# Performance work log

Hardware: AMD Instinct MI355X
Metric: run time of the kernel (lower is better)

Reference implementation:

```python
import jax, jax.numpy as jnp
import numpy as np

NEG_SLOPE = 0.2  # PyG GATConv default negative_slope
EPS = 1e-16


def gat_conv(x, src, dst, num_nodes, W, a_src, a_dst, bias, heads, out_c, concat):
    """PyG-style GATConv (eval mode, self-loops already appended).
    x: [N, F_in]; src/dst: [E] (edge j->i with src=j, dst=i).
    W: [F_in, heads*out_c]; a_src/a_dst: [heads, out_c]; bias: [heads*out_c] or [out_c].
    """
    xw = (x @ W).reshape(num_nodes, heads, out_c)          # [N, H, C]
    alpha_src = jnp.sum(xw * a_src, axis=-1)               # [N, H]
    alpha_dst = jnp.sum(xw * a_dst, axis=-1)               # [N, H]
    e = jax.nn.leaky_relu(alpha_src[src] + alpha_dst[dst], NEG_SLOPE)  # [E, H]
    # numerically stable segment softmax over edges grouped by destination node
    m = jax.ops.segment_max(e, dst, num_segments=num_nodes)            # [N, H]
    e = jnp.exp(e - m[dst])
    denom = jax.ops.segment_sum(e, dst, num_segments=num_nodes)        # [N, H]
    alpha = e / (denom[dst] + EPS)                                     # [E, H]
    # weighted scatter-sum aggregation of source messages
    out = jax.ops.segment_sum(xw[src] * alpha[:, :, None], dst, num_segments=num_nodes)  # [N, H, C]
    if concat:
        out = out.reshape(num_nodes, heads * out_c)
    else:
        out = out.mean(axis=1)
    return out + bias


def setup_inputs() -> dict:
    key = jax.random.key(0)
    ks = jax.random.split(key, 12)
    N, E = 50000, 800000
    F_in, Hid, H1, Out = 512, 32, 8, 64

    def xavier(k, shape, gain=1.414):
        fan_in, fan_out = shape[0], shape[-1] if len(shape) == 2 else int(np.prod(shape[1:]))
        a = gain * np.sqrt(6.0 / (fan_in + fan_out))
        return jax.random.uniform(k, shape, jnp.float32, -a, a)

    x = jax.random.normal(ks[0], (N, F_in), jnp.float32)
    edge_index = jax.random.randint(ks[1], (2, E), 0, N, jnp.int64)

    W1 = xavier(ks[2], (F_in, H1 * Hid))
    a_src1 = xavier(ks[3], (H1, Hid))
    a_dst1 = xavier(ks[4], (H1, Hid))
    b1 = jnp.zeros((H1 * Hid,), jnp.float32)

    W2 = xavier(ks[5], (H1 * Hid, Out))
    a_src2 = xavier(ks[6], (1, Out))
    a_dst2 = xavier(ks[7], (1, Out))
    b2 = jnp.zeros((Out,), jnp.float32)

    return {"x": x, "edge_index": edge_index,
            "W1": W1, "a_src1": a_src1, "a_dst1": a_dst1, "b1": b1,
            "W2": W2, "a_src2": a_src2, "a_dst2": a_dst2, "b2": b2}


def reference(x, edge_index, W1, a_src1, a_dst1, b1, W2, a_src2, a_dst2, b2):
    N = x.shape[0]
    # add self-loops (PyG GATConv default add_self_loops=True)
    loop = jnp.arange(N, dtype=edge_index.dtype)
    src = jnp.concatenate([edge_index[0], loop])
    dst = jnp.concatenate([edge_index[1], loop])

    # eval mode: all dropouts are identity
    h = gat_conv(x, src, dst, N, W1, a_src1, a_dst1, b1, heads=8, out_c=32, concat=True)
    h = jax.nn.elu(h)
    h = gat_conv(h, src, dst, N, W2, a_src2, a_dst2, b2, heads=1, out_c=64, concat=False)
    return jax.nn.log_softmax(h, axis=1)
```

## Files before the change

kernel.cpp:

```cpp
#include <hip/hip_runtime.h>


typedef __attribute__((ext_vector_type(8)))  __bf16          bf16x8;
typedef __attribute__((ext_vector_type(8)))  unsigned short  ushort8;
typedef __attribute__((ext_vector_type(16))) float           f32x16;

#define NEG_SLOPE 0.2f
#define EPS_GAT 1e-16f

static __device__ __forceinline__ float lrelu(float x) {
    return x > 0.0f ? x : NEG_SLOPE * x;
}
static __device__ __forceinline__ unsigned short f2bf(float f) {
    unsigned u = __float_as_uint(f);
    return (unsigned short)((u + 0x7fffu + ((u >> 16) & 1u)) >> 16);
}
static __device__ __forceinline__ float bf2f(unsigned short v) {
    return __uint_as_float(((unsigned)v) << 16);
}

__global__ void k_flag(const unsigned* __restrict__ p, unsigned* sentinel, int E) {
    __shared__ int anynz;
    if (threadIdx.x == 0) anynz = 0;
    __syncthreads();
    int i = threadIdx.x;
    unsigned w = (i < E) ? p[2 * i + 1] : 0u;
    if (w != 0u) atomicOr(&anynz, 1);
    __syncthreads();
    if (threadIdx.x == 0 && anynz) *sentinel = 1u;
}

__global__ void k_convert(const void* __restrict__ p, const unsigned* __restrict__ sentinel,
                          int* __restrict__ esrc, int* __restrict__ edst,
                          int* __restrict__ counts, int E) {
    int i = blockIdx.x * 256 + threadIdx.x;
    if (i >= 2 * E) return;
    bool is64 = (*sentinel == 0u);
    int v = is64 ? (int)((const long long*)p)[i] : ((const int*)p)[i];
    if (i < E) {
        esrc[i] = v;
    } else {
        edst[i - E] = v;
        atomicAdd(&counts[v], 1);
    }
}

__global__ void k_scan1(const int* __restrict__ counts, int* __restrict__ rowp,
                        int* __restrict__ bsum, int N) {
    __shared__ int s[256];
    int t = threadIdx.x, i = blockIdx.x * 256 + t;
    int v = (i < N) ? counts[i] : 0;
    s[t] = v;
    __syncthreads();
    for (int off = 1; off < 256; off <<= 1) {
        int u = (t >= off) ? s[t - off] : 0;
        __syncthreads();
        s[t] += u;
        __syncthreads();
    }
    if (i < N) rowp[i] = s[t] - v;
    if (t == 255) bsum[blockIdx.x] = s[255];
}

__global__ void k_scan2(const int* __restrict__ bsum, int* __restrict__ boff,
                        int* __restrict__ rowp_last, int NB) {
    __shared__ int s[256];
    int t = threadIdx.x;
    int v = (t < NB) ? bsum[t] : 0;
    s[t] = v;
    __syncthreads();
    for (int off = 1; off < 256; off <<= 1) {
        int u = (t >= off) ? s[t - off] : 0;
        __syncthreads();
        s[t] += u;
        __syncthreads();
    }
    if (t < NB) boff[t] = s[t] - v;
    if (t == 255) *rowp_last = s[255];
}

__global__ void k_scan3(int* __restrict__ rowp, int* __restrict__ cursor,
                        const int* __restrict__ boff, int N) {
    int i = blockIdx.x * 256 + threadIdx.x;
    if (i < N) {
        int r = rowp[i] + boff[blockIdx.x];
        rowp[i] = r;
        cursor[i] = r;
    }
}

__global__ void k_fill(const int* __restrict__ esrc, const int* __restrict__ edst,
                       int* __restrict__ cursor, int* __restrict__ sorted_src, int E) {
    int i = blockIdx.x * 256 + threadIdx.x;
    if (i >= E) return;
    int d = edst[i];
    int pos = atomicAdd(&cursor[d], 1);
    sorted_src[pos] = esrc[i];
}

__global__ void k_prep_w(const float* __restrict__ W1, const float* __restrict__ W2,
                         unsigned short* __restrict__ w1t, unsigned short* __restrict__ w2t) {
    int t = blockIdx.x * 256 + threadIdx.x;
    if (t < 512 * 256) {
        int k = t >> 8, m = t & 255;
        w1t[m * 512 + k] = f2bf(W1[t]);
    } else {
        int u = t - 512 * 256;
        if (u < 256 * 64) {
            int k = u >> 6, m = u & 63;
            w2t[m * 256 + k] = f2bf(W2[u]);
        }
    }
}

template <int BM, int BN, int NT, bool AF32, bool OUTBF>
__global__ __launch_bounds__(NT) void k_gemm(const void* __restrict__ Ain,
                                             const unsigned short* __restrict__ Bt,
                                             void* __restrict__ Cout, int Nrows, int K) {
    constexpr int LD = 40;
    __shared__ __align__(16) unsigned short As[BM * LD];
    __shared__ __align__(16) unsigned short Bs[BN * LD];
    const int tid = threadIdx.x;
    const int blockRow = blockIdx.x * BM;
    const int wave = tid >> 6, lane = tid & 63;
    constexpr int WR = BM / 64;
    const int wr = wave % WR, wc = wave / WR;
    const int m = lane & 31;
    const int ksel = (lane >> 5) * 8;

    f32x16 acc00{}, acc01{}, acc10{}, acc11{};

    for (int kt = 0; kt < K; kt += 32) {
        if constexpr (AF32) {
            const float* A = (const float*)Ain;
            for (int idx = tid; idx < BM * 4; idx += NT) {
                int r = idx >> 2, kc = (idx & 3) * 8;
                int grow = blockRow + r;
                float v[8];
                if (grow < Nrows) {
                    const float* ap = A + (size_t)grow * K + kt + kc;
                    float4 x0 = *(const float4*)ap;
                    float4 x1 = *(const float4*)(ap + 4);
                    v[0]=x0.x; v[1]=x0.y; v[2]=x0.z; v[3]=x0.w;
                    v[4]=x1.x; v[5]=x1.y; v[6]=x1.z; v[7]=x1.w;
                } else {
                    #pragma unroll
                    for (int t = 0; t < 8; ++t) v[t] = 0.0f;
                }
                ushort8 o;
                #pragma unroll
                for (int t = 0; t < 8; ++t) o[t] = f2bf(v[t]);
                *(ushort8*)&As[r * LD + kc] = o;
            }
        } else {
            const unsigned short* A = (const unsigned short*)Ain;
            for (int idx = tid; idx < BM * 4; idx += NT) {
                int r = idx >> 2, kc = (idx & 3) * 8;
                int grow = blockRow + r;
                ushort8 o{};
                if (grow < Nrows) o = *(const ushort8*)(A + (size_t)grow * K + kt + kc);
                *(ushort8*)&As[r * LD + kc] = o;
            }
        }
        for (int idx = tid; idx < BN * 4; idx += NT) {
            int r = idx >> 2, kc = (idx & 3) * 8;
            *(ushort8*)&Bs[r * LD + kc] = *(const ushort8*)(Bt + (size_t)r * K + kt + kc);
        }
        __syncthreads();

        #pragma unroll
        for (int kk = 0; kk < 32; kk += 16) {
            bf16x8 a0 = *(const bf16x8*)&As[(wr * 64 +      m) * LD + kk + ksel];
            bf16x8 a1 = *(const bf16x8*)&As[(wr * 64 + 32 + m) * LD + kk + ksel];
            bf16x8 b0 = *(const bf16x8*)&Bs[(wc * 64 +      m) * LD + kk + ksel];
            bf16x8 b1 = *(const bf16x8*)&Bs[(wc * 64 + 32 + m) * LD + kk + ksel];
            acc00 = __builtin_amdgcn_mfma_f32_32x32x16_bf16(a0, b0, acc00, 0, 0, 0);
            acc01 = __builtin_amdgcn_mfma_f32_32x32x16_bf16(a0, b1, acc01, 0, 0, 0);
            acc10 = __builtin_amdgcn_mfma_f32_32x32x16_bf16(a1, b0, acc10, 0, 0, 0);
            acc11 = __builtin_amdgcn_mfma_f32_32x32x16_bf16(a1, b1, acc11, 0, 0, 0);
        }
        __syncthreads();
    }

    const int dcol = wc * 64 + (lane & 31);
    const int dquad = 4 * (lane >> 5);
    auto store_tile = [&](const f32x16& a, int rt, int ct) {
        #pragma unroll
        for (int r = 0; r < 16; ++r) {
            int row = blockRow + wr * 64 + rt * 32 + (r & 3) + 8 * (r >> 2) + dquad;
            if (row < Nrows) {
                size_t off = (size_t)row * BN + dcol + ct * 32;
                if constexpr (OUTBF) ((unsigned short*)Cout)[off] = f2bf(a[r]);
                else                 ((float*)Cout)[off] = a[r];
            }
        }
    };
    store_tile(acc00, 0, 0); store_tile(acc01, 0, 1);
    store_tile(acc10, 1, 0); store_tile(acc11, 1, 1);
}

__global__ void k_alpha(const unsigned short* __restrict__ xw, const float* __restrict__ a_s,
                        const float* __restrict__ a_d, float* __restrict__ os,
                        float* __restrict__ od, float* __restrict__ pmax,
                        int NH, int H, int C) {
    __shared__ float red[256];
    int t = blockIdx.x * 256 + threadIdx.x;
    float s = -1e30f, d = 0.f;
    if (t < NH) {
        int n = t / H, h = t - n * H;
        const unsigned short* row = xw + (size_t)n * H * C + h * C;
        s = 0.f;
        for (int c = 0; c < C; c += 8) {
            ushort8 v = *(const ushort8*)(row + c);
            #pragma unroll
            for (int q = 0; q < 8; ++q) {
                float f = bf2f(v[q]);
                s += f * a_s[h * C + c + q];
                d += f * a_d[h * C + c + q];
            }
        }
        os[t] = s; od[t] = d;
    }
    red[threadIdx.x] = s;
    __syncthreads();
    for (int off = 128; off >= H; off >>= 1) {
        if (threadIdx.x < off) red[threadIdx.x] = fmaxf(red[threadIdx.x], red[threadIdx.x + off]);
        __syncthreads();
    }
    if ((int)threadIdx.x < H) pmax[blockIdx.x * H + threadIdx.x] = red[threadIdx.x];
}

__global__ void k_maxred(const float* __restrict__ partial, int nB, int H,
                         float* __restrict__ M) {
    __shared__ float red[256];
    int t = threadIdx.x;
    int h = t & (H - 1);
    float m = -1e30f;
    for (int b = t / H; b < nB; b += 256 / H)
        m = fmaxf(m, partial[b * H + h]);
    red[t] = m;
    __syncthreads();
    for (int off = 128; off >= H; off >>= 1) {
        if (t < off) red[t] = fmaxf(red[t], red[t + off]);
        __syncthreads();
    }
    if (t < H) M[t] = red[t];
}

__global__ __launch_bounds__(256) void k_agg_l1(
        const unsigned short* __restrict__ xw1, const float* __restrict__ asrc,
        const float* __restrict__ adst, const float* __restrict__ Mh,
        const float* __restrict__ b1, const int* __restrict__ rp,
        const int* __restrict__ ssrc, unsigned short* __restrict__ hbf, int N) {
    int wid = (blockIdx.x * 256 + threadIdx.x) >> 6;
    if (wid >= N) return;
    int lane = threadIdx.x & 63;
    int half = lane >> 5;
    int q    = lane & 31;
    int f0   = q * 8;
    int h    = q >> 2;
    int ih   = wid * 8 + h;
    float ad = adst[ih];
    float m  = lrelu(Mh[h] + ad);
    float acc[8];
    float s;
    {
        float w = (half == 0) ? __expf(lrelu(asrc[ih] + ad) - m) : 0.0f;
        ushort8 xv = *(const ushort8*)(xw1 + (size_t)wid * 256 + f0);
        s = w;
        #pragma unroll
        for (int i = 0; i < 8; ++i) acc[i] = w * bf2f(xv[i]);
    }
    int e0 = rp[wid], e1 = rp[wid + 1];
    if (e0 < e1) {
        int ei = e0 + half;
        bool v_c = ei < e1;
        int j_c = ssrc[v_c ? ei : e1 - 1];
        float as_c = asrc[j_c * 8 + h];
        ushort8 xv_c = *(const ushort8*)(xw1 + (size_t)j_c * 256 + f0);
        for (int e = e0 + 2;; e += 2) {
            bool more = e < e1;
            bool v_n = false;
            float as_n;
            ushort8 xv_n;
            if (more) {
                int en = e + half;
                v_n = en < e1;
                int j_n = ssrc[v_n ? en : e1 - 1];
                as_n = asrc[j_n * 8 + h];
                xv_n = *(const ushort8*)(xw1 + (size_t)j_n * 256 + f0);
            }
            float w = v_c ? __expf(lrelu(as_c + ad) - m) : 0.0f;
            s += w;
            #pragma unroll
            for (int i = 0; i < 8; ++i) acc[i] += w * bf2f(xv_c[i]);
            if (!more) break;
            v_c = v_n; as_c = as_n; xv_c = xv_n;
        }
    }
    s += __shfl_xor(s, 32, 64);
    #pragma unroll
    for (int i = 0; i < 8; ++i) acc[i] += __shfl_xor(acc[i], 32, 64);
    float inv = 1.0f / (s + EPS_GAT);
    int fw = f0 + half * 4;
    ushort4 o;
    #pragma unroll
    for (int i = 0; i < 4; ++i) {
        float v = acc[half * 4 + i] * inv + b1[fw + i];
        v = v > 0.f ? v : expm1f(v);
        ((unsigned short*)&o)[i] = f2bf(v);
    }
    *(ushort4*)(hbf + (size_t)wid * 256 + fw) = o;
}

__global__ __launch_bounds__(256) void k_agg_l2(
        const unsigned short* __restrict__ xw2, const float* __restrict__ asrc,
        const float* __restrict__ adst, const float* __restrict__ Mh,
        const float* __restrict__ b2, const int* __restrict__ rp,
        const int* __restrict__ ssrc, float* __restrict__ out, int N) {
    int wid = (blockIdx.x * 256 + threadIdx.x) >> 6;
    if (wid >= N) return;
    int lane = threadIdx.x & 63;
    int g  = lane >> 4;
    int q  = lane & 15;
    int f0 = q * 4;
    float ad = adst[wid];
    float m = lrelu(Mh[0] + ad);
    float acc[4];
    float s;
    {
        float w = (g == 0) ? __expf(lrelu(asrc[wid] + ad) - m) : 0.0f;
        ushort4 xv = *(const ushort4*)(xw2 + (size_t)wid * 64 + f0);
        s = w;
        acc[0] = w * bf2f(xv.x); acc[1] = w * bf2f(xv.y);
        acc[2] = w * bf2f(xv.z); acc[3] = w * bf2f(xv.w);
    }
    int e0 = rp[wid], e1 = rp[wid + 1];
    if (e0 < e1) {
        int ei = e0 + g;
        bool v_c = ei < e1;
        int j_c = ssrc[v_c ? ei : e1 - 1];
        float as_c = asrc[j_c];
        ushort4 xv_c = *(const ushort4*)(xw2 + (size_t)j_c * 64 + f0);
        for (int e = e0 + 4;; e += 4) {
            bool more = e < e1;
            bool v_n = false;
            float as_n;
            ushort4 xv_n;
            if (more) {
                int en = e + g;
                v_n = en < e1;
                int j_n = ssrc[v_n ? en : e1 - 1];
                as_n = asrc[j_n];
                xv_n = *(const ushort4*)(xw2 + (size_t)j_n * 64 + f0);
            }
            float w = v_c ? __expf(lrelu(as_c + ad) - m) : 0.0f;
            s += w;
            acc[0] += w * bf2f(xv_c.x); acc[1] += w * bf2f(xv_c.y);
            acc[2] += w * bf2f(xv_c.z); acc[3] += w * bf2f(xv_c.w);
            if (!more) break;
            v_c = v_n; as_c = as_n; xv_c = xv_n;
        }
    }
    s += __shfl_xor(s, 16, 64);
    s += __shfl_xor(s, 32, 64);
    #pragma unroll
    for (int i = 0; i < 4; ++i) {
        acc[i] += __shfl_xor(acc[i], 16, 64);
        acc[i] += __shfl_xor(acc[i], 32, 64);
    }
    float inv = 1.0f / (s + EPS_GAT);
    float val[4];
    float mx = -1e30f;
    #pragma unroll
    for (int i = 0; i < 4; ++i) {
        val[i] = acc[i] * inv + b2[f0 + i];
        mx = fmaxf(mx, val[i]);
    }
    #pragma unroll
    for (int off = 8; off > 0; off >>= 1) mx = fmaxf(mx, __shfl_xor(mx, off, 64));
    float sm = 0.f;
    #pragma unroll
    for (int i = 0; i < 4; ++i) sm += __expf(val[i] - mx);
    #pragma unroll
    for (int off = 8; off > 0; off >>= 1) sm += __shfl_xor(sm, off, 64);
    float lse = mx + logf(sm);
    if (g == 0) {
        float4 o = make_float4(val[0] - lse, val[1] - lse, val[2] - lse, val[3] - lse);
        *(float4*)(out + (size_t)wid * 64 + f0) = o;
    }
}

static inline int cdiv(int a, int b) { return (a + b - 1) / b; }

extern "C" void kernel_launch(void* const* d_in, const int* in_sizes, int n_in,
                              void* d_out, int out_size, void* d_ws, size_t ws_size,
                              hipStream_t stream) {
    const float* x   = (const float*)d_in[0];
    const void*  eix = d_in[1];
    const float* W1  = (const float*)d_in[2];
    const float* as1 = (const float*)d_in[3];
    const float* ad1 = (const float*)d_in[4];
    const float* b1  = (const float*)d_in[5];
    const float* W2  = (const float*)d_in[6];
    const float* as2 = (const float*)d_in[7];
    const float* ad2 = (const float*)d_in[8];
    const float* b2  = (const float*)d_in[9];
    float* out = (float*)d_out;

    const int N = in_sizes[0] / 512;
    const int E = in_sizes[1] / 2;
    const int NB = cdiv(N, 256);
    const int NB1 = cdiv(N * 8, 256);
    const int NB2 = cdiv(N, 256);
    (void)n_in; (void)out_size; (void)ws_size;

    char* base = (char*)d_ws;
    size_t o = 0;
    auto alloc = [&](size_t bytes) -> char* {
        o = (o + 255) & ~(size_t)255;
        char* p = base + o;
        o += bytes;
        return p;
    };
    unsigned short* xw1b  = (unsigned short*)alloc((size_t)N * 256 * 2);
    unsigned short* hbf   = (unsigned short*)alloc((size_t)N * 256 * 2);
    unsigned short* xw2b  = (unsigned short*)alloc((size_t)N * 64 * 2);
    float*          asrc1 = (float*)alloc((size_t)N * 8 * 4);
    float*          adst1 = (float*)alloc((size_t)N * 8 * 4);
    float*          asrc2 = (float*)alloc((size_t)N * 4);
    float*          adst2 = (float*)alloc((size_t)N * 4);
    float*          pmax1 = (float*)alloc((size_t)NB1 * 8 * 4);
    float*          pmax2 = (float*)alloc((size_t)NB2 * 4);
    float*          M1    = (float*)alloc(8 * 4);
    float*          M2    = (float*)alloc(4);
    unsigned short* w1t   = (unsigned short*)alloc(512 * 256 * 2);
    unsigned short* w2t   = (unsigned short*)alloc(256 * 64 * 2);
    int*            counts= (int*)alloc((size_t)N * 4);
    int*            cursor= (int*)alloc((size_t)N * 4);
    int*            rowp  = (int*)alloc((size_t)(N + 1) * 4);
    int*            bsum  = (int*)alloc(256 * 4);
    int*            boff  = (int*)alloc(256 * 4);
    int*            esrc  = (int*)alloc((size_t)E * 4);
    int*            edst  = (int*)alloc((size_t)E * 4);
    int*            ssrc  = (int*)alloc((size_t)E * 4);
    unsigned*       sent  = (unsigned*)alloc(256);

    hipMemsetAsync(sent, 0, 4, stream);
    hipMemsetAsync(counts, 0, (size_t)N * 4, stream);

    k_flag<<<1, 256, 0, stream>>>((const unsigned*)eix, sent, E);
    k_convert<<<cdiv(2 * E, 256), 256, 0, stream>>>(eix, sent, esrc, edst, counts, E);
    k_scan1<<<NB, 256, 0, stream>>>(counts, rowp, bsum, N);
    k_scan2<<<1, 256, 0, stream>>>(bsum, boff, rowp + N, NB);
    k_scan3<<<NB, 256, 0, stream>>>(rowp, cursor, boff, N);
    k_fill<<<cdiv(E, 256), 256, 0, stream>>>(esrc, edst, cursor, ssrc, E);

    k_prep_w<<<cdiv(512 * 256 + 256 * 64, 256), 256, 0, stream>>>(W1, W2, w1t, w2t);

    k_gemm<128, 256, 512, true, true><<<cdiv(N, 128), 512, 0, stream>>>(x, w1t, xw1b, N, 512);
    k_alpha<<<NB1, 256, 0, stream>>>(xw1b, as1, ad1, asrc1, adst1, pmax1, N * 8, 8, 32);
    k_maxred<<<1, 256, 0, stream>>>(pmax1, NB1, 8, M1);
    k_agg_l1<<<cdiv(N * 64, 256), 256, 0, stream>>>(xw1b, asrc1, adst1, M1, b1,
                                                    rowp, ssrc, hbf, N);
    k_gemm<256, 64, 256, false, true><<<cdiv(N, 256), 256, 0, stream>>>(hbf, w2t, xw2b, N, 256);
    k_alpha<<<NB2, 256, 0, stream>>>(xw2b, as2, ad2, asrc2, adst2, pmax2, N, 1, 64);
    k_maxred<<<1, 256, 0, stream>>>(pmax2, NB2, 1, M2);
    k_agg_l2<<<cdiv(N * 64, 256), 256, 0, stream>>>(xw2b, asrc2, adst2, M2, b2,
                                                    rowp, ssrc, out, N);
}
```

Before: 449.1 us.

## Fuse max reduction via atomics, deepen gather prefetch, use packed bf16 conversion

Replaces the separate global-max reduction kernels with order-preserving encoded atomicMax inside the alpha kernels, removing two launches. The layer-1 aggregation now processes four edges in parallel per wave, with 16 features per lane and a two-deep prefetch of gathered rows. Layer 2 gains the same two-stage prefetch. The GEMM's fp32-to-bf16 conversion uses packed intrinsics. The deeper prefetch raises register pressure, and the extra shuffles add reduction cost.

```diff
diff --git a/kernel.cpp b/kernel.cpp
--- a/kernel.cpp
+++ b/kernel.cpp
@@ -1,4 +1,5 @@
 #include <hip/hip_runtime.h>
+#include <hip/hip_bf16.h>
 
 
 typedef __attribute__((ext_vector_type(8)))  __bf16          bf16x8;
@@ -17,6 +18,14 @@
 }
 static __device__ __forceinline__ float bf2f(unsigned short v) {
     return __uint_as_float(((unsigned)v) << 16);
+}
+static __device__ __forceinline__ unsigned encf(float x) {
+    unsigned u = __float_as_uint(x);
+    return (u >> 31) ? ~u : (u | 0x80000000u);
+}
+static __device__ __forceinline__ float decf(unsigned e) {
+    unsigned u = (e >> 31) ? (e & 0x7fffffffu) : ~e;
+    return __uint_as_float(u);
 }
 
 __global__ void k_flag(const unsigned* __restrict__ p, unsigned* sentinel, int E) {
@@ -136,21 +145,19 @@
             for (int idx = tid; idx < BM * 4; idx += NT) {
                 int r = idx >> 2, kc = (idx & 3) * 8;
                 int grow = blockRow + r;
-                float v[8];
+                union { ushort8 u; __hip_bfloat162 h[4]; } cv;
                 if (grow < Nrows) {
                     const float* ap = A + (size_t)grow * K + kt + kc;
                     float4 x0 = *(const float4*)ap;
                     float4 x1 = *(const float4*)(ap + 4);
-                    v[0]=x0.x; v[1]=x0.y; v[2]=x0.z; v[3]=x0.w;
-                    v[4]=x1.x; v[5]=x1.y; v[6]=x1.z; v[7]=x1.w;
+                    cv.h[0] = __float22bfloat162_rn(make_float2(x0.x, x0.y));
+                    cv.h[1] = __float22bfloat162_rn(make_float2(x0.z, x0.w));
+                    cv.h[2] = __float22bfloat162_rn(make_float2(x1.x, x1.y));
+                    cv.h[3] = __float22bfloat162_rn(make_float2(x1.z, x1.w));
                 } else {
-                    #pragma unroll
-                    for (int t = 0; t < 8; ++t) v[t] = 0.0f;
+                    cv.u = ushort8{};
                 }
-                ushort8 o;
-                #pragma unroll
-                for (int t = 0; t < 8; ++t) o[t] = f2bf(v[t]);
-                *(ushort8*)&As[r * LD + kc] = o;
+                *(ushort8*)&As[r * LD + kc] = cv.u;
             }
         } else {
             const unsigned short* A = (const unsigned short*)Ain;
@@ -201,7 +208,7 @@
 
 __global__ void k_alpha(const unsigned short* __restrict__ xw, const float* __restrict__ a_s,
                         const float* __restrict__ a_d, float* __restrict__ os,
-                        float* __restrict__ od, float* __restrict__ pmax,
+                        float* __restrict__ od, unsigned* __restrict__ Menc,
                         int NH, int H, int C) {
     __shared__ float red[256];
     int t = blockIdx.x * 256 + threadIdx.x;
@@ -227,86 +234,82 @@
         if (threadIdx.x < off) red[threadIdx.x] = fmaxf(red[threadIdx.x], red[threadIdx.x + off]);
         __syncthreads();
     }
-    if ((int)threadIdx.x < H) pmax[blockIdx.x * H + threadIdx.x] = red[threadIdx.x];
-}
-
-__global__ void k_maxred(const float* __restrict__ partial, int nB, int H,
-                         float* __restrict__ M) {
-    __shared__ float red[256];
-    int t = threadIdx.x;
-    int h = t & (H - 1);
-    float m = -1e30f;
-    for (int b = t / H; b < nB; b += 256 / H)
-        m = fmaxf(m, partial[b * H + h]);
-    red[t] = m;
-    __syncthreads();
-    for (int off = 128; off >= H; off >>= 1) {
-        if (t < off) red[t] = fmaxf(red[t], red[t + off]);
-        __syncthreads();
-    }
-    if (t < H) M[t] = red[t];
+    if ((int)threadIdx.x < H) atomicMax(&Menc[threadIdx.x], encf(red[threadIdx.x]));
 }
 
 __global__ __launch_bounds__(256) void k_agg_l1(
         const unsigned short* __restrict__ xw1, const float* __restrict__ asrc,
-        const float* __restrict__ adst, const float* __restrict__ Mh,
+        const float* __restrict__ adst, const unsigned* __restrict__ Menc,
         const float* __restrict__ b1, const int* __restrict__ rp,
         const int* __restrict__ ssrc, unsigned short* __restrict__ hbf, int N) {
     int wid = (blockIdx.x * 256 + threadIdx.x) >> 6;
     if (wid >= N) return;
     int lane = threadIdx.x & 63;
-    int half = lane >> 5;
-    int q    = lane & 31;
-    int f0   = q * 8;
-    int h    = q >> 2;
-    int ih   = wid * 8 + h;
+    int g  = lane >> 4;
+    int q  = lane & 15;
+    int f0 = q * 16;
+    int h  = q >> 1;
+    int ih = wid * 8 + h;
     float ad = adst[ih];
-    float m  = lrelu(Mh[h] + ad);
-    float acc[8];
+    float m  = lrelu(decf(Menc[h]) + ad);
+    float acc[16];
     float s;
     {
-        float w = (half == 0) ? __expf(lrelu(asrc[ih] + ad) - m) : 0.0f;
-        ushort8 xv = *(const ushort8*)(xw1 + (size_t)wid * 256 + f0);
+        float w = (g == 0) ? __expf(lrelu(asrc[ih] + ad) - m) : 0.0f;
+        const unsigned short* rowp_ = xw1 + (size_t)wid * 256 + f0;
+        ushort8 lo = *(const ushort8*)rowp_;
+        ushort8 hi = *(const ushort8*)(rowp_ + 8);
         s = w;
         #pragma unroll
-        for (int i = 0; i < 8; ++i) acc[i] = w * bf2f(xv[i]);
+        for (int i = 0; i < 8; ++i) { acc[i] = w * bf2f(lo[i]); acc[8 + i] = w * bf2f(hi[i]); }
     }
     int e0 = rp[wid], e1 = rp[wid + 1];
     if (e0 < e1) {
-        int ei = e0 + half;
-        bool v_c = ei < e1;
-        int j_c = ssrc[v_c ? ei : e1 - 1];
-        float as_c = asrc[j_c * 8 + h];
-        ushort8 xv_c = *(const ushort8*)(xw1 + (size_t)j_c * 256 + f0);
-        for (int e = e0 + 2;; e += 2) {
-            bool more = e < e1;
-            bool v_n = false;
-            float as_n;
-            ushort8 xv_n;
-            if (more) {
-                int en = e + half;
-                v_n = en < e1;
-                int j_n = ssrc[v_n ? en : e1 - 1];
-                as_n = asrc[j_n * 8 + h];
-                xv_n = *(const ushort8*)(xw1 + (size_t)j_n * 256 + f0);
-            }
-            float w = v_c ? __expf(lrelu(as_c + ad) - m) : 0.0f;
+        auto loadSlot = [&](int ebase, float& as, ushort8& lo, ushort8& hi, bool& val) {
+            int ei = ebase + g;
+            val = ei < e1;
+            int j = ssrc[val ? ei : e1 - 1];
+            as = asrc[j * 8 + h];
+            const unsigned short* rp_ = xw1 + (size_t)j * 256 + f0;
+            lo = *(const ushort8*)rp_;
+            hi = *(const ushort8*)(rp_ + 8);
+        };
+        float asA; ushort8 loA, hiA; bool vA;
+        loadSlot(e0, asA, loA, hiA, vA);
+        float asB = 0.f; ushort8 loB{}, hiB{}; bool vB = false;
+        bool moreB = e0 + 4 < e1;
+        if (moreB) loadSlot(e0 + 4, asB, loB, hiB, vB);
+        for (int e = e0;;) {
+            float asC = 0.f; ushort8 loC{}, hiC{}; bool vC = false;
+            bool moreC = e + 8 < e1;
+            if (moreC) loadSlot(e + 8, asC, loC, hiC, vC);
+            float w = vA ? __expf(lrelu(asA + ad) - m) : 0.0f;
             s += w;
             #pragma unroll
-            for (int i = 0; i < 8; ++i) acc[i] += w * bf2f(xv_c[i]);
-            if (!more) break;
-            v_c = v_n; as_c = as_n; xv_c = xv_n;
-        }
-    }
+            for (int i = 0; i < 8; ++i) {
+                acc[i]     += w * bf2f(loA[i]);
+                acc[8 + i] += w * bf2f(hiA[i]);
+            }
+            if (!moreB) break;
+            asA = asB; loA = loB; hiA = hiB; vA = vB;
+            asB = asC; loB = loC; hiB = hiC; vB = vC;
+            moreB = moreC;
+            e += 4;
+        }
+    }
+    s += __shfl_xor(s, 16, 64);
     s += __shfl_xor(s, 32, 64);
     #pragma unroll
-    for (int i = 0; i < 8; ++i) acc[i] += __shfl_xor(acc[i], 32, 64);
+    for (int i = 0; i < 16; ++i) {
+        acc[i] += __shfl_xor(acc[i], 16, 64);
+        acc[i] += __shfl_xor(acc[i], 32, 64);
+    }
     float inv = 1.0f / (s + EPS_GAT);
-    int fw = f0 + half * 4;
+    int fw = f0 + g * 4;
     ushort4 o;
     #pragma unroll
     for (int i = 0; i < 4; ++i) {
-        float v = acc[half * 4 + i] * inv + b1[fw + i];
+        float v = acc[g * 4 + i] * inv + b1[fw + i];
         v = v > 0.f ? v : expm1f(v);
         ((unsigned short*)&o)[i] = f2bf(v);
     }
@@ -315,7 +318,7 @@
 
 __global__ __launch_bounds__(256) void k_agg_l2(
         const unsigned short* __restrict__ xw2, const float* __restrict__ asrc,
-        const float* __restrict__ adst, const float* __restrict__ Mh,
+        const float* __restrict__ adst, const unsigned* __restrict__ Menc,
         const float* __restrict__ b2, const int* __restrict__ rp,
         const int* __restrict__ ssrc, float* __restrict__ out, int N) {
     int wid = (blockIdx.x * 256 + threadIdx.x) >> 6;
@@ -325,7 +328,7 @@
     int q  = lane & 15;
     int f0 = q * 4;
     float ad = adst[wid];
-    float m = lrelu(Mh[0] + ad);
+    float m = lrelu(decf(Menc[0]) + ad);
     float acc[4];
     float s;
     {
@@ -337,29 +340,31 @@
     }
     int e0 = rp[wid], e1 = rp[wid + 1];
     if (e0 < e1) {
-        int ei = e0 + g;
-        bool v_c = ei < e1;
-        int j_c = ssrc[v_c ? ei : e1 - 1];
-        float as_c = asrc[j_c];
-        ushort4 xv_c = *(const ushort4*)(xw2 + (size_t)j_c * 64 + f0);
-        for (int e = e0 + 4;; e += 4) {
-            bool more = e < e1;
-            bool v_n = false;
-            float as_n;
-            ushort4 xv_n;
-            if (more) {
-                int en = e + g;
-                v_n = en < e1;
-                int j_n = ssrc[v_n ? en : e1 - 1];
-                as_n = asrc[j_n];
-                xv_n = *(const ushort4*)(xw2 + (size_t)j_n * 64 + f0);
-            }
-            float w = v_c ? __expf(lrelu(as_c + ad) - m) : 0.0f;
+        auto loadSlot = [&](int ebase, float& as, ushort4& xv, bool& val) {
+            int ei = ebase + g;
+            val = ei < e1;
+            int j = ssrc[val ? ei : e1 - 1];
+            as = asrc[j];
+            xv = *(const ushort4*)(xw2 + (size_t)j * 64 + f0);
+        };
+        float asA; ushort4 xvA; bool vA;
+        loadSlot(e0, asA, xvA, vA);
+        float asB = 0.f; ushort4 xvB = {0, 0, 0, 0}; bool vB = false;
+        bool moreB = e0 + 4 < e1;
+        if (moreB) loadSlot(e0 + 4, asB, xvB, vB);
+        for (int e = e0;;) {
+            float asC = 0.f; ushort4 xvC = {0, 0, 0, 0}; bool vC = false;
+            bool moreC = e + 8 < e1;
+            if (moreC) loadSlot(e + 8, asC, xvC, vC);
+            float w = vA ? __expf(lrelu(asA + ad) - m) : 0.0f;
             s += w;
-            acc[0] += w * bf2f(xv_c.x); acc[1] += w * bf2f(xv_c.y);
-            acc[2] += w * bf2f(xv_c.z); acc[3] += w * bf2f(xv_c.w);
-            if (!more) break;
-            v_c = v_n; as_c = as_n; xv_c = xv_n;
+            acc[0] += w * bf2f(xvA.x); acc[1] += w * bf2f(xvA.y);
+            acc[2] += w * bf2f(xvA.z); acc[3] += w * bf2f(xvA.w);
+            if (!moreB) break;
+            asA = asB; xvA = xvB; vA = vB;
+            asB = asC; xvB = xvC; vB = vC;
+            moreB = moreC;
+            e += 4;
         }
     }
     s += __shfl_xor(s, 16, 64);
@@ -430,10 +435,7 @@
     float*          adst1 = (float*)alloc((size_t)N * 8 * 4);
     float*          asrc2 = (float*)alloc((size_t)N * 4);
     float*          adst2 = (float*)alloc((size_t)N * 4);
-    float*          pmax1 = (float*)alloc((size_t)NB1 * 8 * 4);
-    float*          pmax2 = (float*)alloc((size_t)NB2 * 4);
-    float*          M1    = (float*)alloc(8 * 4);
-    float*          M2    = (float*)alloc(4);
+    unsigned*       Menc  = (unsigned*)alloc(16 * 4);
     unsigned short* w1t   = (unsigned short*)alloc(512 * 256 * 2);
     unsigned short* w2t   = (unsigned short*)alloc(256 * 64 * 2);
     int*            counts= (int*)alloc((size_t)N * 4);
@@ -447,6 +449,7 @@
     unsigned*       sent  = (unsigned*)alloc(256);
 
     hipMemsetAsync(sent, 0, 4, stream);
+    hipMemsetAsync(Menc, 0, 16 * 4, stream);
     hipMemsetAsync(counts, 0, (size_t)N * 4, stream);
 
     k_flag<<<1, 256, 0, stream>>>((const unsigned*)eix, sent, E);
@@ -459,13 +462,11 @@
     k_prep_w<<<cdiv(512 * 256 + 256 * 64, 256), 256, 0, stream>>>(W1, W2, w1t, w2t);
 
     k_gemm<128, 256, 512, true, true><<<cdiv(N, 128), 512, 0, stream>>>(x, w1t, xw1b, N, 512);
-    k_alpha<<<NB1, 256, 0, stream>>>(xw1b, as1, ad1, asrc1, adst1, pmax1, N * 8, 8, 32);
-    k_maxred<<<1, 256, 0, stream>>>(pmax1, NB1, 8, M1);
-    k_agg_l1<<<cdiv(N * 64, 256), 256, 0, stream>>>(xw1b, asrc1, adst1, M1, b1,
+    k_alpha<<<NB1, 256, 0, stream>>>(xw1b, as1, ad1, asrc1, adst1, Menc, N * 8, 8, 32);
+    k_agg_l1<<<cdiv(N * 64, 256), 256, 0, stream>>>(xw1b, asrc1, adst1, Menc, b1,
                                                     rowp, ssrc, hbf, N);
     k_gemm<256, 64, 256, false, true><<<cdiv(N, 256), 256, 0, stream>>>(hbf, w2t, xw2b, N, 256);
-    k_alpha<<<NB2, 256, 0, stream>>>(xw2b, as2, ad2, asrc2, adst2, pmax2, N, 1, 64);
-    k_maxred<<<1, 256, 0, stream>>>(pmax2, NB2, 1, M2);
-    k_agg_l2<<<cdiv(N * 64, 256), 256, 0, stream>>>(xw2b, asrc2, adst2, M2, b2,
+    k_alpha<<<NB2, 256, 0, stream>>>(xw2b, as2, ad2, asrc2, adst2, Menc + 8, N, 1, 64);
+    k_agg_l2<<<cdiv(N * 64, 256), 256, 0, stream>>>(xw2b, asrc2, adst2, Menc + 8, b2,
                                                     rowp, ssrc, out, N);
 }
```

Result: faster. 438.5 us (-2.4%).
